# Kernel optimization log

Measured on AMD Instinct MI355X. Metric: run time of the kernel, lower is better.

The kernel has to match this reference:

```python
import jax, jax.numpy as jnp
import numpy as np

DIM = 1024
NH = 16
HD = DIM // NH
EPS = 1e-5


def setup_inputs() -> dict:
    key = jax.random.key(0)
    ks = jax.random.split(key, 6)
    B, LQ, LK = 8, 512, 1024
    s = 1.0 / np.sqrt(DIM)
    return {
        "text_tokens": jax.random.normal(ks[0], (B, LQ, DIM), dtype=jnp.float32),
        "vision_tokens": jax.random.normal(ks[1], (B, LK, DIM), dtype=jnp.float32),
        "in_proj_w": jax.random.normal(ks[2], (3 * DIM, DIM), dtype=jnp.float32) * s,
        "in_proj_b": jnp.zeros((3 * DIM,), dtype=jnp.float32),
        "out_w": jax.random.normal(ks[3], (DIM, DIM), dtype=jnp.float32) * s,
        "out_b": jnp.zeros((DIM,), dtype=jnp.float32),
        "ln_g": jnp.ones((DIM,), dtype=jnp.float32),
        "ln_b": jnp.zeros((DIM,), dtype=jnp.float32),
    }


def _layernorm(x, g, b):
    mu = jnp.mean(x, axis=-1, keepdims=True)
    var = jnp.mean(jnp.square(x - mu), axis=-1, keepdims=True)
    return (x - mu) * jax.lax.rsqrt(var + EPS) * g + b


def reference(text_tokens, vision_tokens, in_proj_w, in_proj_b, out_w, out_b, ln_g, ln_b):
    B, LQ, _ = text_tokens.shape
    LK = vision_tokens.shape[1]
    wq, wk, wv = in_proj_w[:DIM], in_proj_w[DIM:2 * DIM], in_proj_w[2 * DIM:]
    bq, bk, bv = in_proj_b[:DIM], in_proj_b[DIM:2 * DIM], in_proj_b[2 * DIM:]
    q = (text_tokens @ wq.T + bq).reshape(B, LQ, NH, HD)
    k = (vision_tokens @ wk.T + bk).reshape(B, LK, NH, HD)
    v = (vision_tokens @ wv.T + bv).reshape(B, LK, NH, HD)
    scale = 1.0 / np.sqrt(HD)
    scores = jnp.einsum("bqhd,bkhd->bhqk", q, k) * scale  # [B,H,LQ,LK]
    probs = jax.nn.softmax(scores, axis=-1)
    ctx = jnp.einsum("bhqk,bkhd->bqhd", probs, v).reshape(B, LQ, DIM)
    attended = ctx @ out_w.T + out_b
    out = _layernorm(attended + text_tokens, ln_g, ln_b)
    attn_weights = jnp.mean(probs, axis=1)  # PyTorch average_attn_weights=True
    return out, attn_weights
```

## Files before the change

kernel.cpp:

```cpp
#include <hip/hip_runtime.h>

#define DIMV 1024
#define NHV  16
#define HDV  64
#define BV   8
#define LQV  512
#define LKV  1024
#define PSTR 1032

typedef __bf16 bfrag  __attribute__((ext_vector_type(8)));
typedef float  f32x4  __attribute__((ext_vector_type(4)));
typedef unsigned short u16;
typedef unsigned int   u32;
typedef unsigned long long u64;

typedef const __attribute__((address_space(1))) u32 gu32;
typedef __attribute__((address_space(3))) u32 lu32;

__device__ __forceinline__ u16 f2bf(float f) {
    u32 x = __builtin_bit_cast(u32, f);
    x = x + 0x7FFFu + ((x >> 16) & 1u);
    return (u16)(x >> 16);
}

__device__ __forceinline__ void g2l16(const u16* g, const u16* l) {
    __builtin_amdgcn_global_load_lds(
        reinterpret_cast<gu32*>(reinterpret_cast<u64>(g)),
        reinterpret_cast<lu32*>((u32)reinterpret_cast<u64>(l)),
        16, 0, 0);
}

__global__ __launch_bounds__(256)
void cast_bf(const float* __restrict__ src, u16* __restrict__ dst, int n4)
{
    const int i = blockIdx.x * 256 + threadIdx.x;
    if (i < n4) {
        const float4 v = reinterpret_cast<const float4*>(src)[i];
        ushort4 o;
        o.x = f2bf(v.x); o.y = f2bf(v.y); o.z = f2bf(v.z); o.w = f2bf(v.w);
        reinterpret_cast<ushort4*>(dst)[i] = o;
    }
}

template<int MODE>
__global__ __launch_bounds__(256)
void gemm_nt(const u16* __restrict__ A, const u16* __restrict__ W,
             const float* __restrict__ bias, void* __restrict__ Cout,
             const float* __restrict__ resid)
{
    __shared__ __align__(16) u16 sA[128 * 64];
    __shared__ __align__(16) u16 sB[128 * 64];

    const int t    = threadIdx.x;
    const int lane = t & 63;
    const int w    = t >> 6;
    const int quad = lane >> 4;
    const int r    = lane & 15;
    const int wr   = (w >> 1) * 64;
    const int wc   = (w & 1) * 64;
    const int mb   = blockIdx.x * 128;
    const int nb   = blockIdx.y * 128;

    const int srow  = lane >> 3;
    const int skoff = (lane & 7) * 8;

    f32x4 acc[4][4] = {};

    const u16* Abase = A + (size_t)mb * 1024 + skoff;
    const u16* Wbase = W + (size_t)nb * 1024 + skoff;

    for (int k0 = 0; k0 < 1024; k0 += 64) {
#pragma unroll
        for (int it = 0; it < 4; ++it) {
            const int c = w * 4 + it;
            const int row = c * 8 + srow;
            g2l16(Abase + (size_t)row * 1024 + k0, sA + c * 512);
            g2l16(Wbase + (size_t)row * 1024 + k0, sB + c * 512);
        }
        __syncthreads();
#pragma unroll
        for (int kk = 0; kk < 2; ++kk) {
            bfrag af[4], bg[4];
#pragma unroll
            for (int i = 0; i < 4; ++i)
                af[i] = *reinterpret_cast<const bfrag*>(sA + (wr + i * 16 + r) * 64 + kk * 32 + quad * 8);
#pragma unroll
            for (int j = 0; j < 4; ++j)
                bg[j] = *reinterpret_cast<const bfrag*>(sB + (wc + j * 16 + r) * 64 + kk * 32 + quad * 8);
#pragma unroll
            for (int i = 0; i < 4; ++i)
#pragma unroll
                for (int j = 0; j < 4; ++j)
                    acc[i][j] = __builtin_amdgcn_mfma_f32_16x16x32_bf16(af[i], bg[j], acc[i][j], 0, 0, 0);
        }
        __syncthreads();
    }

#pragma unroll
    for (int i = 0; i < 4; i++)
#pragma unroll
    for (int j = 0; j < 4; j++) {
        const int colg = nb + wc + j * 16 + r;
        const float bv = bias[colg];
#pragma unroll
        for (int reg = 0; reg < 4; reg++) {
            const int rowg = mb + wr + i * 16 + quad * 4 + reg;
            const float v = acc[i][j][reg] + bv;
            if (MODE == 0) {
                ((u16*)Cout)[(size_t)rowg * 1024 + colg] = f2bf(v);
            } else if (MODE == 1) {
                ((u16*)Cout)[((size_t)((rowg >> 10) << 10) + colg) * 1024 + (rowg & 1023)] = f2bf(v);
            } else {
                ((float*)Cout)[(size_t)rowg * 1024 + colg] = v + resid[(size_t)rowg * 1024 + colg];
            }
        }
    }
}

__global__ __launch_bounds__(512, 2)
void attn_kernel(const u16* __restrict__ q, const u16* __restrict__ k,
                 const u16* __restrict__ vT, u16* __restrict__ ctx,
                 float* __restrict__ attnw)
{
    __shared__ __align__(16) u16 sP[2][16 * PSTR];
    __shared__ float redm[2][64];
    __shared__ float reds[2][64];

    const int t    = threadIdx.x;
    const int g    = t >> 8;
    const int tg   = t & 255;
    const int lane = tg & 63;
    const int w    = tg >> 6;
    const int quad = lane >> 4;
    const int r    = lane & 15;
    const int b    = blockIdx.y;
    const int q0   = blockIdx.x * 16;

    const int row16 = quad * 4;
    const float scale = 0.125f;

    f32x4 wacc[16] = {};

    for (int hh = 0; hh < 8; ++hh) {
        const int h = g * 8 + hh;
        const int dbase = h * HDV + quad * 8;

        const u16* qp = q + (size_t)(b * LQV + q0 + r) * DIMV + dbase;
        const bfrag qa0 = *reinterpret_cast<const bfrag*>(qp);
        const bfrag qa1 = *reinterpret_cast<const bfrag*>(qp + 32);

        f32x4 s[16];
#pragma unroll
        for (int i = 0; i < 16; ++i) {
            const int n0 = w * 256 + i * 16;
            const u16* kp = k + (size_t)(b * LKV + n0 + r) * DIMV + dbase;
            const bfrag kb0 = *reinterpret_cast<const bfrag*>(kp);
            const bfrag kb1 = *reinterpret_cast<const bfrag*>(kp + 32);
            f32x4 a = {};
            a    = __builtin_amdgcn_mfma_f32_16x16x32_bf16(qa0, kb0, a, 0, 0, 0);
            s[i] = __builtin_amdgcn_mfma_f32_16x16x32_bf16(qa1, kb1, a, 0, 0, 0);
        }

        float mw[4] = {-1e30f, -1e30f, -1e30f, -1e30f};
#pragma unroll
        for (int i = 0; i < 16; ++i)
#pragma unroll
            for (int reg = 0; reg < 4; ++reg) {
                s[i][reg] *= scale;
                mw[reg] = fmaxf(mw[reg], s[i][reg]);
            }
#pragma unroll
        for (int reg = 0; reg < 4; ++reg)
#pragma unroll
            for (int off = 1; off < 16; off <<= 1)
                mw[reg] = fmaxf(mw[reg], __shfl_xor(mw[reg], off));

        float sw[4] = {0.f, 0.f, 0.f, 0.f};
#pragma unroll
        for (int i = 0; i < 16; ++i)
#pragma unroll
            for (int reg = 0; reg < 4; ++reg) {
                s[i][reg] = __expf(s[i][reg] - mw[reg]);
                sw[reg] += s[i][reg];
            }
#pragma unroll
        for (int reg = 0; reg < 4; ++reg)
#pragma unroll
            for (int off = 1; off < 16; off <<= 1)
                sw[reg] += __shfl_xor(sw[reg], off);

        if (r == 0) {
#pragma unroll
            for (int reg = 0; reg < 4; ++reg) {
                redm[g][w * 16 + row16 + reg] = mw[reg];
                reds[g][w * 16 + row16 + reg] = sw[reg];
            }
        }
        __syncthreads();

        float factor[4];
#pragma unroll
        for (int reg = 0; reg < 4; ++reg) {
            const int rr = row16 + reg;
            const float m0 = redm[g][rr], m1 = redm[g][16 + rr], m2 = redm[g][32 + rr], m3 = redm[g][48 + rr];
            const float M = fmaxf(fmaxf(m0, m1), fmaxf(m2, m3));
            const float total = __expf(m0 - M) * reds[g][rr]      + __expf(m1 - M) * reds[g][16 + rr] +
                                __expf(m2 - M) * reds[g][32 + rr] + __expf(m3 - M) * reds[g][48 + rr];
            factor[reg] = __expf(mw[reg] - M) / total;
        }

#pragma unroll
        for (int i = 0; i < 16; ++i)
#pragma unroll
            for (int reg = 0; reg < 4; ++reg) {
                const float pn = s[i][reg] * factor[reg];
                wacc[i][reg] += pn;
                sP[g][(row16 + reg) * PSTR + w * 256 + i * 16 + r] = f2bf(pn);
            }
        __syncthreads();

        {
            const int n0 = w * 16;
            f32x4 c0 = {}, c1 = {}, c2 = {}, c3 = {};
            const u16* vb = vT + (size_t)(b * DIMV + h * HDV + n0 + r) * LKV;
#pragma unroll
            for (int kk = 0; kk < LKV; kk += 128) {
                const bfrag a0 = *reinterpret_cast<const bfrag*>(&sP[g][r * PSTR + kk      + quad * 8]);
                const bfrag a1 = *reinterpret_cast<const bfrag*>(&sP[g][r * PSTR + kk + 32 + quad * 8]);
                const bfrag a2 = *reinterpret_cast<const bfrag*>(&sP[g][r * PSTR + kk + 64 + quad * 8]);
                const bfrag a3 = *reinterpret_cast<const bfrag*>(&sP[g][r * PSTR + kk + 96 + quad * 8]);
                const bfrag b0 = *reinterpret_cast<const bfrag*>(vb + kk      + quad * 8);
                const bfrag b1 = *reinterpret_cast<const bfrag*>(vb + kk + 32 + quad * 8);
                const bfrag b2 = *reinterpret_cast<const bfrag*>(vb + kk + 64 + quad * 8);
                const bfrag b3 = *reinterpret_cast<const bfrag*>(vb + kk + 96 + quad * 8);
                c0 = __builtin_amdgcn_mfma_f32_16x16x32_bf16(a0, b0, c0, 0, 0, 0);
                c1 = __builtin_amdgcn_mfma_f32_16x16x32_bf16(a1, b1, c1, 0, 0, 0);
                c2 = __builtin_amdgcn_mfma_f32_16x16x32_bf16(a2, b2, c2, 0, 0, 0);
                c3 = __builtin_amdgcn_mfma_f32_16x16x32_bf16(a3, b3, c3, 0, 0, 0);
            }
            const f32x4 c = (c0 + c1) + (c2 + c3);
#pragma unroll
            for (int reg = 0; reg < 4; ++reg)
                ctx[(size_t)(b * LQV + q0 + row16 + reg) * DIMV + h * HDV + n0 + r] = f2bf(c[reg]);
        }
        __syncthreads();
    }

    float* cb = reinterpret_cast<float*>(&sP[0][0]);
    if (g == 1) {
#pragma unroll
        for (int i = 0; i < 16; ++i)
#pragma unroll
            for (int reg = 0; reg < 4; ++reg)
                cb[(i * 4 + reg) * 256 + tg] = wacc[i][reg];
    }
    __syncthreads();
    if (g == 0) {
        const float inv16 = 1.0f / 16.0f;
#pragma unroll
        for (int i = 0; i < 16; ++i)
#pragma unroll
            for (int reg = 0; reg < 4; ++reg) {
                const float v = (wacc[i][reg] + cb[(i * 4 + reg) * 256 + tg]) * inv16;
                attnw[(size_t)(b * LQV + q0 + row16 + reg) * LKV + w * 256 + i * 16 + r] = v;
            }
    }
}

__global__ __launch_bounds__(256)
void ln_kernel(const float* __restrict__ x, const float* __restrict__ g,
               const float* __restrict__ bta, float* __restrict__ out)
{
    __shared__ float red[8];
    const int row = blockIdx.x;
    const int t = threadIdx.x;
    const int w = t >> 6;
    const float4 xv = reinterpret_cast<const float4*>(x + (size_t)row * DIMV)[t];

    float s = xv.x + xv.y + xv.z + xv.w;
#pragma unroll
    for (int off = 32; off; off >>= 1) s += __shfl_down(s, off);
    if ((t & 63) == 0) red[w] = s;
    __syncthreads();
    const float mu = (red[0] + red[1] + red[2] + red[3]) * (1.0f / 1024.0f);

    const float d0 = xv.x - mu, d1 = xv.y - mu, d2 = xv.z - mu, d3 = xv.w - mu;
    float s2 = d0 * d0 + d1 * d1 + d2 * d2 + d3 * d3;
#pragma unroll
    for (int off = 32; off; off >>= 1) s2 += __shfl_down(s2, off);
    if ((t & 63) == 0) red[4 + w] = s2;
    __syncthreads();
    const float var = (red[4] + red[5] + red[6] + red[7]) * (1.0f / 1024.0f);
    const float inv = rsqrtf(var + 1e-5f);

    float4 o;
    const int c = t * 4;
    o.x = d0 * inv * g[c + 0] + bta[c + 0];
    o.y = d1 * inv * g[c + 1] + bta[c + 1];
    o.z = d2 * inv * g[c + 2] + bta[c + 2];
    o.w = d3 * inv * g[c + 3] + bta[c + 3];
    reinterpret_cast<float4*>(out + (size_t)row * DIMV)[t] = o;
}

extern "C" void kernel_launch(void* const* d_in, const int* in_sizes, int n_in,
                              void* d_out, int out_size, void* d_ws, size_t ws_size,
                              hipStream_t stream)
{
    const float* text = (const float*)d_in[0];
    const float* vis  = (const float*)d_in[1];
    const float* wqkv = (const float*)d_in[2];
    const float* bqkv = (const float*)d_in[3];
    const float* outw = (const float*)d_in[4];
    const float* outb = (const float*)d_in[5];
    const float* lng  = (const float*)d_in[6];
    const float* lnb  = (const float*)d_in[7];

    char* ws = (char*)d_ws;
    u16*   vis_bf  = (u16*)(ws);
    u16*   ctxb    = (u16*)(ws);
    u16*   wqkv_bf = (u16*)(ws + (size_t)(16u << 20));
    u16*   outw_bf = (u16*)(ws + (size_t)(22u << 20));
    u16*   qb      = (u16*)(ws + (size_t)(24u << 20));
    u16*   text_bf = (u16*)(ws + (size_t)(32u << 20));
    u16*   kb      = (u16*)(ws + (size_t)(32u << 20));
    float* attb    = (float*)(ws + (size_t)(32u << 20));
    u16*   vTb     = (u16*)(ws + (size_t)(48u << 20));

    float* outp  = (float*)d_out;
    float* attnw = outp + (size_t)4096 * 1024;

    const dim3 blk(256);
    cast_bf<<<dim3(8192), blk, 0, stream>>>(vis,  vis_bf,  8388608 / 4);
    cast_bf<<<dim3(3072), blk, 0, stream>>>(wqkv, wqkv_bf, 3145728 / 4);
    cast_bf<<<dim3(1024), blk, 0, stream>>>(outw, outw_bf, 1048576 / 4);
    cast_bf<<<dim3(4096), blk, 0, stream>>>(text, text_bf, 4194304 / 4);

    gemm_nt<0><<<dim3(32, 8), blk, 0, stream>>>(text_bf, wqkv_bf, bqkv, qb, nullptr);
    gemm_nt<0><<<dim3(64, 8), blk, 0, stream>>>(vis_bf, wqkv_bf + DIMV * DIMV, bqkv + DIMV, kb, nullptr);
    gemm_nt<1><<<dim3(64, 8), blk, 0, stream>>>(vis_bf, wqkv_bf + 2 * DIMV * DIMV, bqkv + 2 * DIMV, vTb, nullptr);
    attn_kernel<<<dim3(32, 8), dim3(512), 0, stream>>>(qb, kb, vTb, ctxb, attnw);
    gemm_nt<2><<<dim3(32, 8), blk, 0, stream>>>(ctxb, outw_bf, outb, attb, text);
    ln_kernel<<<dim3(4096), blk, 0, stream>>>(attb, lng, lnb, outp);
}
```

Before: 382.8 us.

## Software-pipeline next head's QK^T with current head's PV in attention

Restructures the attention head loop so the QK^T MFMAs and softmax reduction for head h+1 are interleaved with the PV MFMAs for head h. The max/sum reduction moves into a helper, and the trailing per-head barrier is dropped. The grid is also transposed so the batch index varies fastest across blocks, which changes block scheduling order and K/V cache locality. The aim is to hide global K/V load latency and MFMA dependency stalls, at the cost of more live registers and a possible occupancy or spill risk.

Result: slower. 511.2 us (+33.5%).

```diff
diff --git a/kernel.cpp b/kernel.cpp
--- a/kernel.cpp
+++ b/kernel.cpp
@@ -117,6 +117,39 @@
     }
 }
 
+__device__ __forceinline__ void sm_reduce(f32x4 (&s)[16], float (&mw)[4], float (&sw)[4])
+{
+    const float scale = 0.125f;
+#pragma unroll
+    for (int reg = 0; reg < 4; ++reg) mw[reg] = -1e30f;
+#pragma unroll
+    for (int i = 0; i < 16; ++i)
+#pragma unroll
+        for (int reg = 0; reg < 4; ++reg) {
+            s[i][reg] *= scale;
+            mw[reg] = fmaxf(mw[reg], s[i][reg]);
+        }
+#pragma unroll
+    for (int reg = 0; reg < 4; ++reg)
+#pragma unroll
+        for (int off = 1; off < 16; off <<= 1)
+            mw[reg] = fmaxf(mw[reg], __shfl_xor(mw[reg], off));
+#pragma unroll
+    for (int reg = 0; reg < 4; ++reg) sw[reg] = 0.f;
+#pragma unroll
+    for (int i = 0; i < 16; ++i)
+#pragma unroll
+        for (int reg = 0; reg < 4; ++reg) {
+            s[i][reg] = __expf(s[i][reg] - mw[reg]);
+            sw[reg] += s[i][reg];
+        }
+#pragma unroll
+    for (int reg = 0; reg < 4; ++reg)
+#pragma unroll
+        for (int off = 1; off < 16; off <<= 1)
+            sw[reg] += __shfl_xor(sw[reg], off);
+}
+
 __global__ __launch_bounds__(512, 2)
 void attn_kernel(const u16* __restrict__ q, const u16* __restrict__ k,
                  const u16* __restrict__ vT, u16* __restrict__ ctx,
@@ -133,61 +166,34 @@
     const int w    = tg >> 6;
     const int quad = lane >> 4;
     const int r    = lane & 15;
-    const int b    = blockIdx.y;
-    const int q0   = blockIdx.x * 16;
+    const int b    = blockIdx.x;
+    const int q0   = blockIdx.y * 16;
 
     const int row16 = quad * 4;
-    const float scale = 0.125f;
 
     f32x4 wacc[16] = {};
-
-    for (int hh = 0; hh < 8; ++hh) {
-        const int h = g * 8 + hh;
-        const int dbase = h * HDV + quad * 8;
-
+    f32x4 s[16];
+    float mw[4], sw[4];
+
+    {
+        const int dbase = (g * 8) * HDV + quad * 8;
         const u16* qp = q + (size_t)(b * LQV + q0 + r) * DIMV + dbase;
         const bfrag qa0 = *reinterpret_cast<const bfrag*>(qp);
         const bfrag qa1 = *reinterpret_cast<const bfrag*>(qp + 32);
-
-        f32x4 s[16];
-#pragma unroll
-        for (int i = 0; i < 16; ++i) {
-            const int n0 = w * 256 + i * 16;
-            const u16* kp = k + (size_t)(b * LKV + n0 + r) * DIMV + dbase;
+#pragma unroll
+        for (int u = 0; u < 16; ++u) {
+            const u16* kp = k + (size_t)(b * LKV + w * 256 + u * 16 + r) * DIMV + dbase;
             const bfrag kb0 = *reinterpret_cast<const bfrag*>(kp);
             const bfrag kb1 = *reinterpret_cast<const bfrag*>(kp + 32);
             f32x4 a = {};
             a    = __builtin_amdgcn_mfma_f32_16x16x32_bf16(qa0, kb0, a, 0, 0, 0);
-            s[i] = __builtin_amdgcn_mfma_f32_16x16x32_bf16(qa1, kb1, a, 0, 0, 0);
-        }
-
-        float mw[4] = {-1e30f, -1e30f, -1e30f, -1e30f};
-#pragma unroll
-        for (int i = 0; i < 16; ++i)
-#pragma unroll
-            for (int reg = 0; reg < 4; ++reg) {
-                s[i][reg] *= scale;
-                mw[reg] = fmaxf(mw[reg], s[i][reg]);
-            }
-#pragma unroll
-        for (int reg = 0; reg < 4; ++reg)
-#pragma unroll
-            for (int off = 1; off < 16; off <<= 1)
-                mw[reg] = fmaxf(mw[reg], __shfl_xor(mw[reg], off));
-
-        float sw[4] = {0.f, 0.f, 0.f, 0.f};
-#pragma unroll
-        for (int i = 0; i < 16; ++i)
-#pragma unroll
-            for (int reg = 0; reg < 4; ++reg) {
-                s[i][reg] = __expf(s[i][reg] - mw[reg]);
-                sw[reg] += s[i][reg];
-            }
-#pragma unroll
-        for (int reg = 0; reg < 4; ++reg)
-#pragma unroll
-            for (int off = 1; off < 16; off <<= 1)
-                sw[reg] += __shfl_xor(sw[reg], off);
+            s[u] = __builtin_amdgcn_mfma_f32_16x16x32_bf16(qa1, kb1, a, 0, 0, 0);
+        }
+        sm_reduce(s, mw, sw);
+    }
+
+    for (int hh = 0; hh < 8; ++hh) {
+        const int h = g * 8 + hh;
 
         if (r == 0) {
 #pragma unroll
@@ -219,12 +225,44 @@
             }
         __syncthreads();
 
-        {
-            const int n0 = w * 16;
-            f32x4 c0 = {}, c1 = {}, c2 = {}, c3 = {};
-            const u16* vb = vT + (size_t)(b * DIMV + h * HDV + n0 + r) * LKV;
-#pragma unroll
-            for (int kk = 0; kk < LKV; kk += 128) {
+        const int n0 = w * 16;
+        const u16* vb = vT + (size_t)(b * DIMV + h * HDV + n0 + r) * LKV;
+        f32x4 c0 = {}, c1 = {}, c2 = {}, c3 = {};
+
+        if (hh < 7) {
+            const int dbase2 = (h + 1) * HDV + quad * 8;
+            const u16* qp2 = q + (size_t)(b * LQV + q0 + r) * DIMV + dbase2;
+            const bfrag qa0 = *reinterpret_cast<const bfrag*>(qp2);
+            const bfrag qa1 = *reinterpret_cast<const bfrag*>(qp2 + 32);
+#pragma unroll
+            for (int u = 0; u < 16; ++u) {
+                const u16* kp = k + (size_t)(b * LKV + w * 256 + u * 16 + r) * DIMV + dbase2;
+                const bfrag kb0 = *reinterpret_cast<const bfrag*>(kp);
+                const bfrag kb1 = *reinterpret_cast<const bfrag*>(kp + 32);
+                f32x4 a = {};
+                a    = __builtin_amdgcn_mfma_f32_16x16x32_bf16(qa0, kb0, a, 0, 0, 0);
+                s[u] = __builtin_amdgcn_mfma_f32_16x16x32_bf16(qa1, kb1, a, 0, 0, 0);
+                if (u < 8) {
+                    const int kk = u * 128;
+                    const bfrag a0 = *reinterpret_cast<const bfrag*>(&sP[g][r * PSTR + kk      + quad * 8]);
+                    const bfrag a1 = *reinterpret_cast<const bfrag*>(&sP[g][r * PSTR + kk + 32 + quad * 8]);
+                    const bfrag a2 = *reinterpret_cast<const bfrag*>(&sP[g][r * PSTR + kk + 64 + quad * 8]);
+                    const bfrag a3 = *reinterpret_cast<const bfrag*>(&sP[g][r * PSTR + kk + 96 + quad * 8]);
+                    const bfrag b0 = *reinterpret_cast<const bfrag*>(vb + kk      + quad * 8);
+                    const bfrag b1 = *reinterpret_cast<const bfrag*>(vb + kk + 32 + quad * 8);
+                    const bfrag b2 = *reinterpret_cast<const bfrag*>(vb + kk + 64 + quad * 8);
+                    const bfrag b3 = *reinterpret_cast<const bfrag*>(vb + kk + 96 + quad * 8);
+                    c0 = __builtin_amdgcn_mfma_f32_16x16x32_bf16(a0, b0, c0, 0, 0, 0);
+                    c1 = __builtin_amdgcn_mfma_f32_16x16x32_bf16(a1, b1, c1, 0, 0, 0);
+                    c2 = __builtin_amdgcn_mfma_f32_16x16x32_bf16(a2, b2, c2, 0, 0, 0);
+                    c3 = __builtin_amdgcn_mfma_f32_16x16x32_bf16(a3, b3, c3, 0, 0, 0);
+                }
+            }
+            sm_reduce(s, mw, sw);
+        } else {
+#pragma unroll
+            for (int u = 0; u < 8; ++u) {
+                const int kk = u * 128;
                 const bfrag a0 = *reinterpret_cast<const bfrag*>(&sP[g][r * PSTR + kk      + quad * 8]);
                 const bfrag a1 = *reinterpret_cast<const bfrag*>(&sP[g][r * PSTR + kk + 32 + quad * 8]);
                 const bfrag a2 = *reinterpret_cast<const bfrag*>(&sP[g][r * PSTR + kk + 64 + quad * 8]);
@@ -238,13 +276,15 @@
                 c2 = __builtin_amdgcn_mfma_f32_16x16x32_bf16(a2, b2, c2, 0, 0, 0);
                 c3 = __builtin_amdgcn_mfma_f32_16x16x32_bf16(a3, b3, c3, 0, 0, 0);
             }
-            const f32x4 c = (c0 + c1) + (c2 + c3);
-#pragma unroll
-            for (int reg = 0; reg < 4; ++reg)
-                ctx[(size_t)(b * LQV + q0 + row16 + reg) * DIMV + h * HDV + n0 + r] = f2bf(c[reg]);
-        }
-        __syncthreads();
-    }
+        }
+
+        const f32x4 c = (c0 + c1) + (c2 + c3);
+#pragma unroll
+        for (int reg = 0; reg < 4; ++reg)
+            ctx[(size_t)(b * LQV + q0 + row16 + reg) * DIMV + h * HDV + n0 + r] = f2bf(c[reg]);
+    }
+
+    __syncthreads();
 
     float* cb = reinterpret_cast<float*>(&sP[0][0]);
     if (g == 1) {
@@ -338,7 +378,7 @@
     gemm_nt<0><<<dim3(32, 8), blk, 0, stream>>>(text_bf, wqkv_bf, bqkv, qb, nullptr);
     gemm_nt<0><<<dim3(64, 8), blk, 0, stream>>>(vis_bf, wqkv_bf + DIMV * DIMV, bqkv + DIMV, kb, nullptr);
     gemm_nt<1><<<dim3(64, 8), blk, 0, stream>>>(vis_bf, wqkv_bf + 2 * DIMV * DIMV, bqkv + 2 * DIMV, vTb, nullptr);
-    attn_kernel<<<dim3(32, 8), dim3(512), 0, stream>>>(qb, kb, vTb, ctxb, attnw);
+    attn_kernel<<<dim3(8, 32), dim3(512), 0, stream>>>(qb, kb, vTb, ctxb, attnw);
     gemm_nt<2><<<dim3(32, 8), blk, 0, stream>>>(ctxb, outw_bf, outb, attb, text);
     ln_kernel<<<dim3(4096), blk, 0, stream>>>(attb, lng, lnb, outp);
 }
```
